# Optimization experiments

Measured on AMD Instinct MI355X. Metric: run time of the kernel, lower is better.

Reference implementation:

```python
import jax
import jax.numpy as jnp
from jax import lax
import numpy as np

N, D, V, T = 16384, 256, 32000, 128
U_DECAY = 0.97


def _ln_row(z, eps=1e-6):
    # torch layernorm_row: (z - mean) / (std_unbiased + eps)
    m = z.mean(axis=-1, keepdims=True)
    s = z.std(axis=-1, ddof=1, keepdims=True)  # torch .std is unbiased
    return (z - m) / (s + eps)


def setup_inputs() -> dict:
    key = jax.random.key(0)
    k0, k1, k2, k3, k4 = jax.random.split(key, 5)
    E = jax.random.normal(k0, (D, N), dtype=jnp.float32) / np.sqrt(N).astype(np.float32)
    Dx = jax.random.normal(k1, (N, D), dtype=jnp.float32) / np.sqrt(D).astype(np.float32)
    Dy = jax.random.normal(k2, (N, D), dtype=jnp.float32) / np.sqrt(D).astype(np.float32)
    token_emb = jax.random.normal(k3, (V, D), dtype=jnp.float32) / np.sqrt(D).astype(np.float32)
    tokens = jax.random.randint(k4, (T,), 0, V)
    return {"E": E, "Dx": Dx, "Dy": Dy, "token_emb": token_emb, "tokens": tokens}


def reference(E, Dx, Dy, token_emb, tokens):
    d, n = E.shape

    def step(carry, tok):
        x, rho = carry
        v_prev = token_emb[tok]                    # [d]
        x_t = x + jax.nn.relu(Dx @ v_prev)         # [n], use_relu_lowrank=True
        a_star = rho @ x_t                         # [d]
        y_core = Dy @ _ln_row(a_star)              # [n], ln_before_Dy=True
        y_t = jax.nn.relu(y_core) * jnp.maximum(x_t, 0.0)
        v_star = _ln_row(E @ y_t)                  # [d]
        rho = U_DECAY * (rho + jnp.outer(v_prev, x_t))  # rank-1 write + decay
        return (x_t, rho), (y_t, v_star)

    x0 = jnp.zeros((n,), dtype=E.dtype)
    rho0 = jnp.zeros((d, n), dtype=E.dtype)
    (x_f, rho_f), (ys, vs) = lax.scan(step, (x0, rho0), tokens)
    # final states x, y, v, rho concatenated into one vector
    return jnp.concatenate([x_f, ys[-1], vs[-1], rho_f.ravel()])
```

## Files before the change

### kernel.cpp

```cpp
#include <hip/hip_runtime.h>
#include <cstddef>

namespace {
constexpr int Nn = 16384;
constexpr int Dd = 256;
constexpr int Tt = 128;
constexpr float DECAY = 0.97f;

constexpr size_t WS_CUMVT = 0;
constexpr size_t WS_VB    = 16384;
constexpr size_t WS_H     = 49152;
constexpr size_t WS_LNA   = 49280;
constexpr size_t WS_U     = 49536;
}

typedef __attribute__((ext_vector_type(8))) short short8;
typedef __attribute__((ext_vector_type(4))) short short4v;
typedef __attribute__((ext_vector_type(4))) float f32x4;
typedef unsigned short u16;

__device__ __forceinline__ u16 f2bf(float f) {
  unsigned u = __builtin_bit_cast(unsigned, f);
  return (u16)((u + 0x7fffu + ((u >> 16) & 1u)) >> 16);
}

__global__ __launch_bounds__(256) void k0(const float* __restrict__ temb,
                                          const int* __restrict__ toks,
                                          u16* __restrict__ cumVT,
                                          float* __restrict__ Vb) {
  __shared__ int st[Tt];
  const int s = blockIdx.x, d = threadIdx.x;
  if (d < Tt) st[d] = toks[d];
  __syncthreads();
  float run = 0.f, w = DECAY, v = 0.f;
  for (int t = Tt - 1; t >= s; --t) {
    v = temb[(size_t)st[t] * Dd + d];
    run += w * v;
    w *= DECAY;
  }
  Vb[s * Dd + d] = v;
  cumVT[d * Tt + s] = f2bf(run);
}

__global__ __launch_bounds__(256) void k_p1(const float* __restrict__ Dx,
                                            const float* __restrict__ Vb,
                                            const u16* __restrict__ cumVT,
                                            float* __restrict__ h,
                                            float* __restrict__ xf,
                                            float* __restrict__ rho) {
  __shared__ __align__(16) u16 Asl[32 * 40];
  __shared__ __align__(16) u16 Bsl[128 * 40];
  __shared__ __align__(16) u16 Mld[32 * 136];
  __shared__ __align__(16) u16 CVl[64 * 136];
  __shared__ float xpart[4][16];
  __shared__ float hpart[4][64];
  __shared__ float xjl[32];

  const int tid = threadIdx.x;
  const int j0 = blockIdx.x * 32;
  const int w = tid >> 6, l = tid & 63;
  const int jt = w & 1, thf = w >> 1;
  const int lr = l & 15, lg = l >> 4;

  const float4* Dx4 = (const float4*)Dx;
  const float4* Vb4 = (const float4*)Vb;

  const int ar = tid >> 3, akq = tid & 7;
  const int btr = tid >> 1, bh = tid & 1;

  f32x4 zero = {0.f, 0.f, 0.f, 0.f};
  f32x4 acc[4] = {zero, zero, zero, zero};

  float4 pa = Dx4[(size_t)(j0 + ar) * 64 + akq];
  float4 pb0 = Vb4[(size_t)btr * 64 + bh * 4 + 0];
  float4 pb1 = Vb4[(size_t)btr * 64 + bh * 4 + 1];
  float4 pb2 = Vb4[(size_t)btr * 64 + bh * 4 + 2];
  float4 pb3 = Vb4[(size_t)btr * 64 + bh * 4 + 3];

  for (int ch = 0; ch < 8; ++ch) {
    __syncthreads();
    {
      short4v a4;
      a4[0] = (short)f2bf(pa.x); a4[1] = (short)f2bf(pa.y);
      a4[2] = (short)f2bf(pa.z); a4[3] = (short)f2bf(pa.w);
      *(short4v*)&Asl[ar * 40 + akq * 4] = a4;
    }
    {
      short8 b0, b1;
      b0[0] = (short)f2bf(pb0.x); b0[1] = (short)f2bf(pb0.y);
      b0[2] = (short)f2bf(pb0.z); b0[3] = (short)f2bf(pb0.w);
      b0[4] = (short)f2bf(pb1.x); b0[5] = (short)f2bf(pb1.y);
      b0[6] = (short)f2bf(pb1.z); b0[7] = (short)f2bf(pb1.w);
      b1[0] = (short)f2bf(pb2.x); b1[1] = (short)f2bf(pb2.y);
      b1[2] = (short)f2bf(pb2.z); b1[3] = (short)f2bf(pb2.w);
      b1[4] = (short)f2bf(pb3.x); b1[5] = (short)f2bf(pb3.y);
      b1[6] = (short)f2bf(pb3.z); b1[7] = (short)f2bf(pb3.w);
      *(short8*)&Bsl[btr * 40 + bh * 16] = b0;
      *(short8*)&Bsl[btr * 40 + bh * 16 + 8] = b1;
    }
    __syncthreads();
    if (ch < 7) {
      pa = Dx4[(size_t)(j0 + ar) * 64 + (ch + 1) * 8 + akq];
      pb0 = Vb4[(size_t)btr * 64 + (ch + 1) * 8 + bh * 4 + 0];
      pb1 = Vb4[(size_t)btr * 64 + (ch + 1) * 8 + bh * 4 + 1];
      pb2 = Vb4[(size_t)btr * 64 + (ch + 1) * 8 + bh * 4 + 2];
      pb3 = Vb4[(size_t)btr * 64 + (ch + 1) * 8 + bh * 4 + 3];
    }
    short8 av = *(const short8*)&Asl[(jt * 16 + lr) * 40 + lg * 8];
#pragma unroll
    for (int tt = 0; tt < 4; ++tt) {
      short8 bv = *(const short8*)&Bsl[((thf * 4 + tt) * 16 + lr) * 40 + lg * 8];
      acc[tt] = __builtin_amdgcn_mfma_f32_16x16x32_bf16(av, bv, acc[tt], 0, 0, 0);
    }
  }

#pragma unroll
  for (int tt = 0; tt < 4; ++tt)
#pragma unroll
    for (int q = 0; q < 4; ++q) {
      float vv = fmaxf(acc[tt][q], 0.f);
      acc[tt][q] = vv;
      Mld[(jt * 16 + lg * 4 + q) * 136 + thf * 64 + tt * 16 + lr] = f2bf(vv);
    }

  float p0 = acc[0][0] + acc[1][0] + acc[2][0] + acc[3][0];
  float p1 = acc[0][1] + acc[1][1] + acc[2][1] + acc[3][1];
  float p2 = acc[0][2] + acc[1][2] + acc[2][2] + acc[3][2];
  float p3 = acc[0][3] + acc[1][3] + acc[2][3] + acc[3][3];
#pragma unroll
  for (int m = 1; m <= 8; m <<= 1) {
    p0 += __shfl_xor(p0, m); p1 += __shfl_xor(p1, m);
    p2 += __shfl_xor(p2, m); p3 += __shfl_xor(p3, m);
  }
  float pv = p0;
  if (lr == 1) pv = p1; else if (lr == 2) pv = p2; else if (lr == 3) pv = p3;
  if (lr < 4) xpart[w][lg * 4 + lr] = pv;
  __syncthreads();
  if (tid < 32) {
    float s = xpart[tid >> 4][tid & 15] + xpart[(tid >> 4) + 2][tid & 15];
    xjl[tid] = s;
    xf[j0 + tid] = s;
  }
  __syncthreads();

  float xq0 = xjl[jt * 16 + lg * 4 + 0];
  float xq1 = xjl[jt * 16 + lg * 4 + 1];
  float xq2 = xjl[jt * 16 + lg * 4 + 2];
  float xq3 = xjl[jt * 16 + lg * 4 + 3];
  float ph0 = acc[0][0]*xq0 + acc[0][1]*xq1 + acc[0][2]*xq2 + acc[0][3]*xq3;
  float ph1 = acc[1][0]*xq0 + acc[1][1]*xq1 + acc[1][2]*xq2 + acc[1][3]*xq3;
  float ph2 = acc[2][0]*xq0 + acc[2][1]*xq1 + acc[2][2]*xq2 + acc[2][3]*xq3;
  float ph3 = acc[3][0]*xq0 + acc[3][1]*xq1 + acc[3][2]*xq2 + acc[3][3]*xq3;
#pragma unroll
  for (int m = 16; m <= 32; m <<= 1) {
    ph0 += __shfl_xor(ph0, m); ph1 += __shfl_xor(ph1, m);
    ph2 += __shfl_xor(ph2, m); ph3 += __shfl_xor(ph3, m);
  }
  if (l < 16) {
    hpart[w][l] = ph0; hpart[w][16 + l] = ph1;
    hpart[w][32 + l] = ph2; hpart[w][48 + l] = ph3;
  }
  __syncthreads();
  if (tid < Tt) {
    int half = tid >> 6;
    atomicAdd(&h[tid], hpart[half * 2][tid & 63] + hpart[half * 2 + 1][tid & 63]);
  }

  const float4* CV4 = (const float4*)cumVT;
  float4 q0 = CV4[tid], q1 = CV4[tid + 256], q2 = CV4[tid + 512],
         q3 = CV4[tid + 768];
  for (int dc = 0; dc < 4; ++dc) {
    __syncthreads();
    *(float4*)&CVl[(tid >> 4) * 136 + (tid & 15) * 8] = q0;
    *(float4*)&CVl[((tid + 256) >> 4) * 136 + (tid & 15) * 8] = q1;
    *(float4*)&CVl[((tid + 512) >> 4) * 136 + (tid & 15) * 8] = q2;
    *(float4*)&CVl[((tid + 768) >> 4) * 136 + (tid & 15) * 8] = q3;
    __syncthreads();
    if (dc < 3) {
      q0 = CV4[(dc + 1) * 1024 + tid];
      q1 = CV4[(dc + 1) * 1024 + tid + 256];
      q2 = CV4[(dc + 1) * 1024 + tid + 512];
      q3 = CV4[(dc + 1) * 1024 + tid + 768];
    }
    f32x4 r0 = zero, r1 = zero;
#pragma unroll
    for (int ks = 0; ks < 4; ++ks) {
      short8 a = *(const short8*)&CVl[(w * 16 + lr) * 136 + ks * 32 + lg * 8];
      short8 b0 = *(const short8*)&Mld[lr * 136 + ks * 32 + lg * 8];
      short8 b1 = *(const short8*)&Mld[(16 + lr) * 136 + ks * 32 + lg * 8];
      r0 = __builtin_amdgcn_mfma_f32_16x16x32_bf16(a, b0, r0, 0, 0, 0);
      r1 = __builtin_amdgcn_mfma_f32_16x16x32_bf16(a, b1, r1, 0, 0, 0);
    }
#pragma unroll
    for (int q = 0; q < 4; ++q) {
      size_t drow = (size_t)(dc * 64 + w * 16 + lg * 4 + q) * Nn;
      rho[drow + j0 + lr] = r0[q];
      rho[drow + j0 + 16 + lr] = r1[q];
    }
  }
}

__global__ __launch_bounds__(256) void k_astar(const float* __restrict__ h,
                                               const float* __restrict__ Vb,
                                               float* __restrict__ lna) {
  __shared__ float g[Tt];
  __shared__ float red[Dd];
  const int d = threadIdx.x;
  if (d < Tt) g[d] = h[d];
  __syncthreads();
  for (int off = 1; off < Tt; off <<= 1) {
    float v = 0.f;
    bool act = (d < Tt) && (d >= off);
    if (act) v = g[d - off];
    __syncthreads();
    if (act) g[d] += v;
    __syncthreads();
  }
  float a = 0.f, wv = DECAY;
  for (int t = Tt - 2; t >= 0; --t) {
    a += wv * g[t] * Vb[t * Dd + d];
    wv *= DECAY;
  }
  red[d] = a;
  __syncthreads();
  for (int off = 128; off > 0; off >>= 1) {
    if (d < off) red[d] += red[d + off];
    __syncthreads();
  }
  float m = red[0] * (1.f / 256.f);
  __syncthreads();
  float c0 = a - m;
  red[d] = c0 * c0;
  __syncthreads();
  for (int off = 128; off > 0; off >>= 1) {
    if (d < off) red[d] += red[d + off];
    __syncthreads();
  }
  float sd = sqrtf(red[0] * (1.f / 255.f));
  lna[d] = c0 / (sd + 1e-6f);
}

__global__ void k_y(const float* __restrict__ Dy, const float* __restrict__ lna,
                    const float* __restrict__ x, float* __restrict__ yout) {
  const int tid = threadIdx.x;
  const int wave = tid >> 6, lane = tid & 63;
  const int j = blockIdx.x * 4 + wave;
  const float4* Dy4 = (const float4*)Dy;
  const float4* l4 = (const float4*)lna;
  float4 a = Dy4[(size_t)j * 64 + lane];
  float4 bq = l4[lane];
  float acc = a.x * bq.x + a.y * bq.y + a.z * bq.z + a.w * bq.w;
#pragma unroll
  for (int off = 32; off > 0; off >>= 1) acc += __shfl_down(acc, off);
  if (lane == 0) yout[j] = fmaxf(acc, 0.f) * fmaxf(x[j], 0.f);
}

__global__ void k_u(const float* __restrict__ E, const float* __restrict__ y,
                    float* __restrict__ u) {
  __shared__ float red[256];
  const int d = blockIdx.x >> 1, hf = blockIdx.x & 1, tid = threadIdx.x;
  const float4* E4 = (const float4*)E;
  const float4* y4 = (const float4*)y;
  float acc = 0.f;
#pragma unroll
  for (int i = 0; i < 8; ++i) {
    int idx = hf * 2048 + tid + i * 256;
    float4 e = E4[(size_t)d * 4096 + idx];
    float4 yv = y4[idx];
    acc += e.x * yv.x + e.y * yv.y + e.z * yv.z + e.w * yv.w;
  }
  red[tid] = acc;
  __syncthreads();
  for (int off = 128; off > 0; off >>= 1) {
    if (tid < off) red[tid] += red[tid + off];
    __syncthreads();
  }
  if (tid == 0) atomicAdd(&u[d], red[0]);
}

__global__ void k_v(const float* __restrict__ u, float* __restrict__ vout) {
  __shared__ float red[256];
  const int d = threadIdx.x;
  float a = u[d];
  red[d] = a;
  __syncthreads();
  for (int off = 128; off > 0; off >>= 1) {
    if (d < off) red[d] += red[d + off];
    __syncthreads();
  }
  float m = red[0] * (1.f / 256.f);
  __syncthreads();
  float c0 = a - m;
  red[d] = c0 * c0;
  __syncthreads();
  for (int off = 128; off > 0; off >>= 1) {
    if (d < off) red[d] += red[d + off];
    __syncthreads();
  }
  float sd = sqrtf(red[0] * (1.f / 255.f));
  vout[d] = c0 / (sd + 1e-6f);
}

extern "C" void kernel_launch(void* const* d_in, const int* in_sizes, int n_in,
                              void* d_out, int out_size, void* d_ws, size_t ws_size,
                              hipStream_t stream) {
  const float* E = (const float*)d_in[0];
  const float* Dx = (const float*)d_in[1];
  const float* Dy = (const float*)d_in[2];
  const float* temb = (const float*)d_in[3];
  const int* toks = (const int*)d_in[4];

  float* ws = (float*)d_ws;
  float* out = (float*)d_out;
  u16* cumVT = (u16*)(ws + WS_CUMVT);
  float* Vb  = ws + WS_VB;
  float* h   = ws + WS_H;
  float* lna = ws + WS_LNA;
  float* u   = ws + WS_U;

  float* xf  = out;
  float* yv  = out + Nn;
  float* vs  = out + 2 * Nn;
  float* rho = out + 2 * Nn + Dd;

  hipMemsetAsync(h, 0, (Tt + 2 * Dd) * sizeof(float), stream);

  k0<<<Tt, 256, 0, stream>>>(temb, toks, cumVT, Vb);
  k_p1<<<Nn / 32, 256, 0, stream>>>(Dx, Vb, cumVT, h, xf, rho);
  k_astar<<<1, 256, 0, stream>>>(h, Vb, lna);
  k_y<<<Nn / 4, 256, 0, stream>>>(Dy, lna, xf, yv);
  k_u<<<2 * Dd, 256, 0, stream>>>(E, yv, u);
  k_v<<<1, 256, 0, stream>>>(u, vs);
}
```

Before: 185.0 us.

## Fuse a_star/LN, y and E@y kernels; precompute bf16 token embeddings and split cumsum

The first kernel is split into a gather kernel, which writes fp32 and bf16 copies of the token embeddings, and a single-block suffix-sum kernel that writes packed bf16 cumulative vectors. This replaces the old per-block O(T) rescans. k_p1 now loads the pre-converted bf16 embeddings directly into shared memory instead of converting them each chunk. The a_star layernorm, the Dy matvec and the E@y reduction are merged into one kernel with 256 blocks, which removes two launches and the workspace round trip. The cost is that every block redundantly recomputes the prefix scan and the a_star layernorm, and the E reduction now issues many more atomics using per-wave shuffle reductions.

Measured after the change: 297.7 us. +60.9%, slower.

```diff
diff --git a/kernel.cpp b/kernel.cpp
--- a/kernel.cpp
+++ b/kernel.cpp
@@ -9,14 +9,15 @@
 
 constexpr size_t WS_CUMVT = 0;
 constexpr size_t WS_VB    = 16384;
-constexpr size_t WS_H     = 49152;
-constexpr size_t WS_LNA   = 49280;
-constexpr size_t WS_U     = 49536;
+constexpr size_t WS_VBBF  = 49152;
+constexpr size_t WS_H     = 65536;
+constexpr size_t WS_U     = 65664;
 }
 
 typedef __attribute__((ext_vector_type(8))) short short8;
 typedef __attribute__((ext_vector_type(4))) short short4v;
 typedef __attribute__((ext_vector_type(4))) float f32x4;
+typedef __attribute__((ext_vector_type(4))) unsigned int u32x4;
 typedef unsigned short u16;
 
 __device__ __forceinline__ u16 f2bf(float f) {
@@ -24,26 +25,38 @@
   return (u16)((u + 0x7fffu + ((u >> 16) & 1u)) >> 16);
 }
 
-__global__ __launch_bounds__(256) void k0(const float* __restrict__ temb,
-                                          const int* __restrict__ toks,
-                                          u16* __restrict__ cumVT,
-                                          float* __restrict__ Vb) {
-  __shared__ int st[Tt];
+__global__ __launch_bounds__(256) void k_gather(const float* __restrict__ temb,
+                                                const int* __restrict__ toks,
+                                                float* __restrict__ Vb,
+                                                u16* __restrict__ VbBf) {
   const int s = blockIdx.x, d = threadIdx.x;
-  if (d < Tt) st[d] = toks[d];
-  __syncthreads();
-  float run = 0.f, w = DECAY, v = 0.f;
-  for (int t = Tt - 1; t >= s; --t) {
-    v = temb[(size_t)st[t] * Dd + d];
-    run += w * v;
+  float v = temb[(size_t)toks[s] * Dd + d];
+  Vb[s * Dd + d] = v;
+  VbBf[s * Dd + d] = f2bf(v);
+}
+
+__global__ __launch_bounds__(256) void k_cumv(const float* __restrict__ Vb,
+                                              u16* __restrict__ cumVT) {
+  const int d = threadIdx.x;
+  float run = 0.f, w = DECAY;
+  unsigned pk[64];
+#pragma unroll
+  for (int t = Tt - 1; t >= 0; --t) {
+    run += w * Vb[t * Dd + d];
     w *= DECAY;
-  }
-  Vb[s * Dd + d] = v;
-  cumVT[d * Tt + s] = f2bf(run);
+    unsigned bb = (unsigned)f2bf(run);
+    if (t & 1) pk[t >> 1] = bb << 16;
+    else       pk[t >> 1] |= bb;
+  }
+#pragma unroll
+  for (int i = 0; i < 16; ++i) {
+    u32x4 o = {pk[4 * i], pk[4 * i + 1], pk[4 * i + 2], pk[4 * i + 3]};
+    *(u32x4*)&cumVT[d * Tt + i * 8] = o;
+  }
 }
 
 __global__ __launch_bounds__(256) void k_p1(const float* __restrict__ Dx,
-                                            const float* __restrict__ Vb,
+                                            const u16* __restrict__ VbBf,
                                             const u16* __restrict__ cumVT,
                                             float* __restrict__ h,
                                             float* __restrict__ xf,
@@ -63,7 +76,7 @@
   const int lr = l & 15, lg = l >> 4;
 
   const float4* Dx4 = (const float4*)Dx;
-  const float4* Vb4 = (const float4*)Vb;
+  const float4* VB4 = (const float4*)VbBf;
 
   const int ar = tid >> 3, akq = tid & 7;
   const int btr = tid >> 1, bh = tid & 1;
@@ -72,10 +85,8 @@
   f32x4 acc[4] = {zero, zero, zero, zero};
 
   float4 pa = Dx4[(size_t)(j0 + ar) * 64 + akq];
-  float4 pb0 = Vb4[(size_t)btr * 64 + bh * 4 + 0];
-  float4 pb1 = Vb4[(size_t)btr * 64 + bh * 4 + 1];
-  float4 pb2 = Vb4[(size_t)btr * 64 + bh * 4 + 2];
-  float4 pb3 = Vb4[(size_t)btr * 64 + bh * 4 + 3];
+  float4 pb0 = VB4[btr * 32 + bh * 2];
+  float4 pb1 = VB4[btr * 32 + bh * 2 + 1];
 
   for (int ch = 0; ch < 8; ++ch) {
     __syncthreads();
@@ -85,26 +96,13 @@
       a4[2] = (short)f2bf(pa.z); a4[3] = (short)f2bf(pa.w);
       *(short4v*)&Asl[ar * 40 + akq * 4] = a4;
     }
-    {
-      short8 b0, b1;
-      b0[0] = (short)f2bf(pb0.x); b0[1] = (short)f2bf(pb0.y);
-      b0[2] = (short)f2bf(pb0.z); b0[3] = (short)f2bf(pb0.w);
-      b0[4] = (short)f2bf(pb1.x); b0[5] = (short)f2bf(pb1.y);
-      b0[6] = (short)f2bf(pb1.z); b0[7] = (short)f2bf(pb1.w);
-      b1[0] = (short)f2bf(pb2.x); b1[1] = (short)f2bf(pb2.y);
-      b1[2] = (short)f2bf(pb2.z); b1[3] = (short)f2bf(pb2.w);
-      b1[4] = (short)f2bf(pb3.x); b1[5] = (short)f2bf(pb3.y);
-      b1[6] = (short)f2bf(pb3.z); b1[7] = (short)f2bf(pb3.w);
-      *(short8*)&Bsl[btr * 40 + bh * 16] = b0;
-      *(short8*)&Bsl[btr * 40 + bh * 16 + 8] = b1;
-    }
+    *(float4*)&Bsl[btr * 40 + bh * 16] = pb0;
+    *(float4*)&Bsl[btr * 40 + bh * 16 + 8] = pb1;
     __syncthreads();
     if (ch < 7) {
       pa = Dx4[(size_t)(j0 + ar) * 64 + (ch + 1) * 8 + akq];
-      pb0 = Vb4[(size_t)btr * 64 + (ch + 1) * 8 + bh * 4 + 0];
-      pb1 = Vb4[(size_t)btr * 64 + (ch + 1) * 8 + bh * 4 + 1];
-      pb2 = Vb4[(size_t)btr * 64 + (ch + 1) * 8 + bh * 4 + 2];
-      pb3 = Vb4[(size_t)btr * 64 + (ch + 1) * 8 + bh * 4 + 3];
+      pb0 = VB4[btr * 32 + (ch + 1) * 4 + bh * 2];
+      pb1 = VB4[btr * 32 + (ch + 1) * 4 + bh * 2 + 1];
     }
     short8 av = *(const short8*)&Asl[(jt * 16 + lr) * 40 + lg * 8];
 #pragma unroll
@@ -200,82 +198,82 @@
   }
 }
 
-__global__ __launch_bounds__(256) void k_astar(const float* __restrict__ h,
-                                               const float* __restrict__ Vb,
-                                               float* __restrict__ lna) {
+__global__ __launch_bounds__(256) void k_yu(const float* __restrict__ Dy,
+                                            const float* __restrict__ E,
+                                            const float* __restrict__ Vb,
+                                            const float* __restrict__ h,
+                                            const float* __restrict__ xf,
+                                            float* __restrict__ yv,
+                                            float* __restrict__ u) {
   __shared__ float g[Tt];
   __shared__ float red[Dd];
-  const int d = threadIdx.x;
-  if (d < Tt) g[d] = h[d];
+  __shared__ float lna_l[Dd];
+  __shared__ float y_l[64];
+  const int tid = threadIdx.x;
+  const int b = blockIdx.x;
+  const int wv = tid >> 6, lane = tid & 63;
+  const int j0 = b * 64;
+
+  if (tid < Tt) g[tid] = h[tid];
   __syncthreads();
   for (int off = 1; off < Tt; off <<= 1) {
-    float v = 0.f;
-    bool act = (d < Tt) && (d >= off);
-    if (act) v = g[d - off];
-    __syncthreads();
-    if (act) g[d] += v;
-    __syncthreads();
-  }
-  float a = 0.f, wv = DECAY;
+    float vsc = 0.f;
+    bool act = (tid < Tt) && (tid >= off);
+    if (act) vsc = g[tid - off];
+    __syncthreads();
+    if (act) g[tid] += vsc;
+    __syncthreads();
+  }
+  float a = 0.f, w = DECAY;
   for (int t = Tt - 2; t >= 0; --t) {
-    a += wv * g[t] * Vb[t * Dd + d];
-    wv *= DECAY;
-  }
-  red[d] = a;
-  __syncthreads();
-  for (int off = 128; off > 0; off >>= 1) {
-    if (d < off) red[d] += red[d + off];
-    __syncthreads();
-  }
-  float m = red[0] * (1.f / 256.f);
-  __syncthreads();
-  float c0 = a - m;
-  red[d] = c0 * c0;
-  __syncthreads();
-  for (int off = 128; off > 0; off >>= 1) {
-    if (d < off) red[d] += red[d + off];
-    __syncthreads();
-  }
-  float sd = sqrtf(red[0] * (1.f / 255.f));
-  lna[d] = c0 / (sd + 1e-6f);
-}
-
-__global__ void k_y(const float* __restrict__ Dy, const float* __restrict__ lna,
-                    const float* __restrict__ x, float* __restrict__ yout) {
-  const int tid = threadIdx.x;
-  const int wave = tid >> 6, lane = tid & 63;
-  const int j = blockIdx.x * 4 + wave;
-  const float4* Dy4 = (const float4*)Dy;
-  const float4* l4 = (const float4*)lna;
-  float4 a = Dy4[(size_t)j * 64 + lane];
-  float4 bq = l4[lane];
-  float acc = a.x * bq.x + a.y * bq.y + a.z * bq.z + a.w * bq.w;
-#pragma unroll
-  for (int off = 32; off > 0; off >>= 1) acc += __shfl_down(acc, off);
-  if (lane == 0) yout[j] = fmaxf(acc, 0.f) * fmaxf(x[j], 0.f);
-}
-
-__global__ void k_u(const float* __restrict__ E, const float* __restrict__ y,
-                    float* __restrict__ u) {
-  __shared__ float red[256];
-  const int d = blockIdx.x >> 1, hf = blockIdx.x & 1, tid = threadIdx.x;
-  const float4* E4 = (const float4*)E;
-  const float4* y4 = (const float4*)y;
-  float acc = 0.f;
-#pragma unroll
-  for (int i = 0; i < 8; ++i) {
-    int idx = hf * 2048 + tid + i * 256;
-    float4 e = E4[(size_t)d * 4096 + idx];
-    float4 yv = y4[idx];
-    acc += e.x * yv.x + e.y * yv.y + e.z * yv.z + e.w * yv.w;
-  }
-  red[tid] = acc;
+    a += w * g[t] * Vb[t * Dd + tid];
+    w *= DECAY;
+  }
+  red[tid] = a;
   __syncthreads();
   for (int off = 128; off > 0; off >>= 1) {
     if (tid < off) red[tid] += red[tid + off];
     __syncthreads();
   }
-  if (tid == 0) atomicAdd(&u[d], red[0]);
+  float m = red[0] * (1.f / 256.f);
+  __syncthreads();
+  float c0 = a - m;
+  red[tid] = c0 * c0;
+  __syncthreads();
+  for (int off = 128; off > 0; off >>= 1) {
+    if (tid < off) red[tid] += red[tid + off];
+    __syncthreads();
+  }
+  float sd = sqrtf(red[0] * (1.f / 255.f));
+  lna_l[tid] = c0 / (sd + 1e-6f);
+  __syncthreads();
+
+  const float4* Dy4 = (const float4*)Dy;
+  const float4* l4 = (const float4*)lna_l;
+  float4 lv = l4[lane];
+  for (int i = 0; i < 16; ++i) {
+    int jl = wv * 16 + i, j = j0 + jl;
+    float4 dv = Dy4[(size_t)j * 64 + lane];
+    float accy = dv.x * lv.x + dv.y * lv.y + dv.z * lv.z + dv.w * lv.w;
+#pragma unroll
+    for (int off = 32; off > 0; off >>= 1) accy += __shfl_down(accy, off);
+    float xv = xf[j];
+    if (lane == 0) {
+      float yy = fmaxf(accy, 0.f) * fmaxf(xv, 0.f);
+      y_l[jl] = yy;
+      yv[j] = yy;
+    }
+  }
+  __syncthreads();
+
+  float yj = y_l[lane];
+  for (int i = 0; i < 64; ++i) {
+    int d = wv * 64 + i;
+    float p = E[(size_t)d * Nn + j0 + lane] * yj;
+#pragma unroll
+    for (int off = 32; off > 0; off >>= 1) p += __shfl_down(p, off);
+    if (lane == 0) atomicAdd(&u[d], p);
+  }
 }
 
 __global__ void k_v(const float* __restrict__ u, float* __restrict__ vout) {
@@ -314,8 +312,8 @@
   float* out = (float*)d_out;
   u16* cumVT = (u16*)(ws + WS_CUMVT);
   float* Vb  = ws + WS_VB;
+  u16* VbBf  = (u16*)(ws + WS_VBBF);
   float* h   = ws + WS_H;
-  float* lna = ws + WS_LNA;
   float* u   = ws + WS_U;
 
   float* xf  = out;
@@ -323,12 +321,11 @@
   float* vs  = out + 2 * Nn;
   float* rho = out + 2 * Nn + Dd;
 
-  hipMemsetAsync(h, 0, (Tt + 2 * Dd) * sizeof(float), stream);
-
-  k0<<<Tt, 256, 0, stream>>>(temb, toks, cumVT, Vb);
-  k_p1<<<Nn / 32, 256, 0, stream>>>(Dx, Vb, cumVT, h, xf, rho);
-  k_astar<<<1, 256, 0, stream>>>(h, Vb, lna);
-  k_y<<<Nn / 4, 256, 0, stream>>>(Dy, lna, xf, yv);
-  k_u<<<2 * Dd, 256, 0, stream>>>(E, yv, u);
+  hipMemsetAsync(h, 0, (Tt + Dd) * sizeof(float), stream);
+
+  k_gather<<<Tt, Dd, 0, stream>>>(temb, toks, Vb, VbBf);
+  k_cumv<<<1, Dd, 0, stream>>>(Vb, cumVT);
+  k_p1<<<Nn / 32, 256, 0, stream>>>(Dx, VbBf, cumVT, h, xf, rho);
+  k_yu<<<Nn / 64, 256, 0, stream>>>(Dy, E, Vb, h, xf, yv, u);
   k_v<<<1, 256, 0, stream>>>(u, vs);
 }
```

## Split token gather from decayed cumulative sum and pre-convert embeddings to bf16

Applied to the files above, without the earlier changes.

The old prologue kernel had each of 128 blocks re-gather the suffix of token embeddings, which is quadratic work. The gather now runs once per token and also writes a bf16 copy. A single-block kernel then computes the decayed suffix sums sequentially and stores them as packed vector writes. The main GEMM kernel reads the pre-converted bf16 embeddings, which removes per-block fp32 loads and conversions. The cost is an extra kernel launch, and the suffix-sum step becomes a serial 128-step loop running in only one block.

Result: faster. 156.2 us (-15.6%).

```diff
diff --git a/kernel.cpp b/kernel.cpp
--- a/kernel.cpp
+++ b/kernel.cpp
@@ -9,14 +9,16 @@
 
 constexpr size_t WS_CUMVT = 0;
 constexpr size_t WS_VB    = 16384;
-constexpr size_t WS_H     = 49152;
-constexpr size_t WS_LNA   = 49280;
-constexpr size_t WS_U     = 49536;
+constexpr size_t WS_VBBF  = 49152;
+constexpr size_t WS_H     = 65536;
+constexpr size_t WS_U     = 65664;
+constexpr size_t WS_LNA   = 65920;
 }
 
 typedef __attribute__((ext_vector_type(8))) short short8;
 typedef __attribute__((ext_vector_type(4))) short short4v;
 typedef __attribute__((ext_vector_type(4))) float f32x4;
+typedef __attribute__((ext_vector_type(4))) unsigned int u32x4;
 typedef unsigned short u16;
 
 __device__ __forceinline__ u16 f2bf(float f) {
@@ -24,26 +26,38 @@
   return (u16)((u + 0x7fffu + ((u >> 16) & 1u)) >> 16);
 }
 
-__global__ __launch_bounds__(256) void k0(const float* __restrict__ temb,
-                                          const int* __restrict__ toks,
-                                          u16* __restrict__ cumVT,
-                                          float* __restrict__ Vb) {
-  __shared__ int st[Tt];
+__global__ __launch_bounds__(256) void k_gather(const float* __restrict__ temb,
+                                                const int* __restrict__ toks,
+                                                float* __restrict__ Vb,
+                                                u16* __restrict__ VbBf) {
   const int s = blockIdx.x, d = threadIdx.x;
-  if (d < Tt) st[d] = toks[d];
-  __syncthreads();
-  float run = 0.f, w = DECAY, v = 0.f;
-  for (int t = Tt - 1; t >= s; --t) {
-    v = temb[(size_t)st[t] * Dd + d];
-    run += w * v;
+  float v = temb[(size_t)toks[s] * Dd + d];
+  Vb[s * Dd + d] = v;
+  VbBf[s * Dd + d] = f2bf(v);
+}
+
+__global__ __launch_bounds__(256) void k_cumv(const float* __restrict__ Vb,
+                                              u16* __restrict__ cumVT) {
+  const int d = threadIdx.x;
+  float run = 0.f, w = DECAY;
+  unsigned pk[64];
+#pragma unroll
+  for (int t = Tt - 1; t >= 0; --t) {
+    run += w * Vb[t * Dd + d];
     w *= DECAY;
-  }
-  Vb[s * Dd + d] = v;
-  cumVT[d * Tt + s] = f2bf(run);
+    unsigned bb = (unsigned)f2bf(run);
+    if (t & 1) pk[t >> 1] = bb << 16;
+    else       pk[t >> 1] |= bb;
+  }
+#pragma unroll
+  for (int i = 0; i < 16; ++i) {
+    u32x4 o = {pk[4 * i], pk[4 * i + 1], pk[4 * i + 2], pk[4 * i + 3]};
+    *(u32x4*)&cumVT[d * Tt + i * 8] = o;
+  }
 }
 
 __global__ __launch_bounds__(256) void k_p1(const float* __restrict__ Dx,
-                                            const float* __restrict__ Vb,
+                                            const u16* __restrict__ VbBf,
                                             const u16* __restrict__ cumVT,
                                             float* __restrict__ h,
                                             float* __restrict__ xf,
@@ -63,7 +77,7 @@
   const int lr = l & 15, lg = l >> 4;
 
   const float4* Dx4 = (const float4*)Dx;
-  const float4* Vb4 = (const float4*)Vb;
+  const float4* VB4 = (const float4*)VbBf;
 
   const int ar = tid >> 3, akq = tid & 7;
   const int btr = tid >> 1, bh = tid & 1;
@@ -72,10 +86,8 @@
   f32x4 acc[4] = {zero, zero, zero, zero};
 
   float4 pa = Dx4[(size_t)(j0 + ar) * 64 + akq];
-  float4 pb0 = Vb4[(size_t)btr * 64 + bh * 4 + 0];
-  float4 pb1 = Vb4[(size_t)btr * 64 + bh * 4 + 1];
-  float4 pb2 = Vb4[(size_t)btr * 64 + bh * 4 + 2];
-  float4 pb3 = Vb4[(size_t)btr * 64 + bh * 4 + 3];
+  float4 pb0 = VB4[btr * 32 + bh * 2];
+  float4 pb1 = VB4[btr * 32 + bh * 2 + 1];
 
   for (int ch = 0; ch < 8; ++ch) {
     __syncthreads();
@@ -85,26 +97,13 @@
       a4[2] = (short)f2bf(pa.z); a4[3] = (short)f2bf(pa.w);
       *(short4v*)&Asl[ar * 40 + akq * 4] = a4;
     }
-    {
-      short8 b0, b1;
-      b0[0] = (short)f2bf(pb0.x); b0[1] = (short)f2bf(pb0.y);
-      b0[2] = (short)f2bf(pb0.z); b0[3] = (short)f2bf(pb0.w);
-      b0[4] = (short)f2bf(pb1.x); b0[5] = (short)f2bf(pb1.y);
-      b0[6] = (short)f2bf(pb1.z); b0[7] = (short)f2bf(pb1.w);
-      b1[0] = (short)f2bf(pb2.x); b1[1] = (short)f2bf(pb2.y);
-      b1[2] = (short)f2bf(pb2.z); b1[3] = (short)f2bf(pb2.w);
-      b1[4] = (short)f2bf(pb3.x); b1[5] = (short)f2bf(pb3.y);
-      b1[6] = (short)f2bf(pb3.z); b1[7] = (short)f2bf(pb3.w);
-      *(short8*)&Bsl[btr * 40 + bh * 16] = b0;
-      *(short8*)&Bsl[btr * 40 + bh * 16 + 8] = b1;
-    }
+    *(float4*)&Bsl[btr * 40 + bh * 16] = pb0;
+    *(float4*)&Bsl[btr * 40 + bh * 16 + 8] = pb1;
     __syncthreads();
     if (ch < 7) {
       pa = Dx4[(size_t)(j0 + ar) * 64 + (ch + 1) * 8 + akq];
-      pb0 = Vb4[(size_t)btr * 64 + (ch + 1) * 8 + bh * 4 + 0];
-      pb1 = Vb4[(size_t)btr * 64 + (ch + 1) * 8 + bh * 4 + 1];
-      pb2 = Vb4[(size_t)btr * 64 + (ch + 1) * 8 + bh * 4 + 2];
-      pb3 = Vb4[(size_t)btr * 64 + (ch + 1) * 8 + bh * 4 + 3];
+      pb0 = VB4[btr * 32 + (ch + 1) * 4 + bh * 2];
+      pb1 = VB4[btr * 32 + (ch + 1) * 4 + bh * 2 + 1];
     }
     short8 av = *(const short8*)&Asl[(jt * 16 + lr) * 40 + lg * 8];
 #pragma unroll
@@ -314,19 +313,21 @@
   float* out = (float*)d_out;
   u16* cumVT = (u16*)(ws + WS_CUMVT);
   float* Vb  = ws + WS_VB;
+  u16* VbBf  = (u16*)(ws + WS_VBBF);
   float* h   = ws + WS_H;
+  float* u   = ws + WS_U;
   float* lna = ws + WS_LNA;
-  float* u   = ws + WS_U;
 
   float* xf  = out;
   float* yv  = out + Nn;
   float* vs  = out + 2 * Nn;
   float* rho = out + 2 * Nn + Dd;
 
-  hipMemsetAsync(h, 0, (Tt + 2 * Dd) * sizeof(float), stream);
-
-  k0<<<Tt, 256, 0, stream>>>(temb, toks, cumVT, Vb);
-  k_p1<<<Nn / 32, 256, 0, stream>>>(Dx, Vb, cumVT, h, xf, rho);
+  hipMemsetAsync(h, 0, (Tt + Dd) * sizeof(float), stream);
+
+  k_gather<<<Tt, Dd, 0, stream>>>(temb, toks, Vb, VbBf);
+  k_cumv<<<1, Dd, 0, stream>>>(Vb, cumVT);
+  k_p1<<<Nn / 32, 256, 0, stream>>>(Dx, VbBf, cumVT, h, xf, rho);
   k_astar<<<1, 256, 0, stream>>>(h, Vb, lna);
   k_y<<<Nn / 4, 256, 0, stream>>>(Dy, lna, xf, yv);
   k_u<<<2 * Dd, 256, 0, stream>>>(E, yv, u);
```
